# Performance work log

Hardware: AMD Instinct MI355X
Metric: run time of the kernel (lower is better)

The kernel has to match this reference:

```python
import jax, jax.numpy as jnp
import numpy as np

# Model constants (match init_kwargs)
H, P, N, G, NL, K = 32, 64, 128, 1, 15, 4   # heads, head_dim, state, groups, lambda levels, conv width
HID, T, BATCH = 1024, 1024, 1
INTER = H * P                    # 2048
CONV_DIM = INTER + 2 * G * N     # 2304
PROJ = INTER + CONV_DIM + H * (NL + 1)  # 4864
EPS = 1e-5


def _level_matrix(t_len: int) -> np.ndarray:
    """Fenwick-tree level assignment: for query t, prefix [0,t] splits into
    power-of-two segments from binary expansion of t+1; segment of length 2^l -> level l."""
    lm = np.zeros((t_len, t_len), dtype=np.int32)
    for t in range(t_len):
        n = t + 1
        while n > 0:
            lb = n & (-n)
            lm[t, n - lb:n] = lb.bit_length() - 1
            n -= lb
    return lm


def setup_inputs() -> dict:
    key = jax.random.key(0)
    ks = jax.random.split(key, 4)
    return {
        "hidden_states": jax.random.normal(ks[0], (BATCH, T, HID), jnp.float32),
        "in_proj_w": jax.random.normal(ks[1], (PROJ, HID), jnp.float32) / np.sqrt(HID).astype(np.float32),
        "in_proj_b": jnp.zeros((PROJ,), jnp.float32),
        "conv_w": jax.random.normal(ks[2], (CONV_DIM, K), jnp.float32) / np.sqrt(K).astype(np.float32),
        "dt_bias": jnp.ones((H,), jnp.float32),
        "A_log": jnp.log(jnp.arange(1, H + 1, dtype=jnp.float32)),
        "L_param": jnp.ones((H, NL), jnp.float32),
        "D": jnp.ones((H,), jnp.float32),
        "rmsnorm_w": jnp.ones((INTER,), jnp.float32),
        "out_proj_w": jax.random.normal(ks[3], (HID, INTER), jnp.float32) / np.sqrt(INTER).astype(np.float32),
        "out_proj_b": jnp.zeros((HID,), jnp.float32),
        "level_mat": jnp.asarray(_level_matrix(T)),  # (T,T) int32, data-independent
    }


def reference(hidden_states, in_proj_w, in_proj_b, conv_w, dt_bias, A_log,
              L_param, D, rmsnorm_w, out_proj_w, out_proj_b, level_mat):
    b, t, _ = hidden_states.shape
    # in_proj and split: [z | xBC | dt | dl]
    zxbcdtdl = hidden_states @ in_proj_w.T + in_proj_b
    z, xBC, dt, dl = jnp.split(zxbcdtdl, [INTER, INTER + CONV_DIM, INTER + CONV_DIM + H], axis=-1)
    # depthwise causal conv1d (width K) + SiLU
    xp = jnp.pad(xBC, ((0, 0), (K - 1, 0), (0, 0)))
    conv = sum(xp[:, w:w + t, :] * conv_w[:, w] for w in range(K))
    xBC = jax.nn.silu(conv)
    x, Bm, Cm = jnp.split(xBC, [INTER, INTER + G * N], axis=-1)
    x = x.reshape(b, t, H, P)          # v pre-scale
    Bm = Bm.reshape(b, t, G, N)        # keys
    Cm = Cm.reshape(b, t, G, N)        # queries
    dl = dl.reshape(b, t, H, NL)
    # D residual uses unscaled x (matches hmamba_chunk_scan_combined ordering)
    D_res = x * D[None, None, :, None]
    dt = jax.nn.softplus(dt + dt_bias)            # (b,t,H)
    v = x * dt[..., None]                          # (b,t,H,P)
    A = -jnp.exp(A_log)                            # (H,)
    g = A * dt                                     # (b,t,H), per-token log-decay (<=0)
    Ls = jax.nn.softplus(L_param * dl)             # (b,t,H,NL) per-token level scales
    # cumulative log-decay; decay(t,s) = exp(cg_t - cg_s), s<=t
    cg = jnp.cumsum(g, axis=1).transpose(0, 2, 1)  # (b,H,t)
    mask = jnp.tril(jnp.ones((t, t), bool))
    logdecay = jnp.where(mask, cg[:, :, :, None] - cg[:, :, None, :], -jnp.inf)
    decay = jnp.exp(logdecay)                      # (b,H,t,s)
    # hierarchical level scale H[t,s] = Ls[b,t,h, level(t,s)]
    Hmat = jnp.take_along_axis(Ls.transpose(0, 2, 1, 3), level_mat[None, None, :, :], axis=-1)  # (b,H,t,s)
    scores = jnp.einsum('btgn,bsgn->bgts', Cm, Bm)  # (b,G,t,s), G=1 broadcasts over heads
    att = scores * decay * Hmat                     # (b,H,t,s), masked via decay=0
    y = jnp.einsum('bhts,bshp->bthp', att, v) + D_res
    y = y.reshape(b, t, INTER)
    # gated RMSNorm with norm_before_gate=False: normalize(y * silu(z)) * w
    yg = y * jax.nn.silu(z)
    y = yg * jax.lax.rsqrt(jnp.mean(yg * yg, axis=-1, keepdims=True) + EPS) * rmsnorm_w
    return y @ out_proj_w.T + out_proj_b
```

## Files before the change

### kernel.cpp

```cpp
#include <hip/hip_runtime.h>
#include <hip/hip_bf16.h>
#include <math.h>

#define T_LEN 1024
#define HID 1024
#define NHEAD 32
#define HDIM 64
#define NSTATE 128
#define NLVL 15
#define KCONV 4
#define INTER 2048
#define CONV_DIM 2304
#define PROJ 4864
#define EPS 1e-5f

typedef __attribute__((ext_vector_type(8))) _Float16 half8;
typedef __attribute__((ext_vector_type(4))) float float4v;
typedef unsigned short ushort_t;

__device__ __forceinline__ float softplus_f(float x) {
  return fmaxf(x, 0.f) + log1pf(expf(-fabsf(x)));
}
__device__ __forceinline__ float silu_f(float x) {
  return x / (1.f + expf(-x));
}
__device__ __forceinline__ ushort_t f2h(float f) {
  union { _Float16 h; ushort_t u; } v;
  v.h = (_Float16)f;
  return v.u;
}
__device__ __forceinline__ void gload_lds16(const void* g, void* l) {
  __builtin_amdgcn_global_load_lds(
      (const __attribute__((address_space(1))) void*)g,
      (__attribute__((address_space(3))) void*)l, 16, 0, 0);
}

#define N4_HS  (T_LEN * HID / 4)
#define N4_WI  (PROJ * HID / 4)
#define N4_WO  (HID * INTER / 4)
__global__ __launch_bounds__(256) void prep_f16(
    const float* __restrict__ hs, const float* __restrict__ wi,
    const float* __restrict__ wo, ushort_t* __restrict__ hsb,
    ushort_t* __restrict__ wib, ushort_t* __restrict__ wob) {
  int i = blockIdx.x * 256 + threadIdx.x;
  const float* src; ushort_t* dst; int j;
  if (i < N4_HS)              { src = hs; dst = hsb; j = i; }
  else if (i < N4_HS + N4_WI) { src = wi; dst = wib; j = i - N4_HS; }
  else                        { src = wo; dst = wob; j = i - N4_HS - N4_WI; }
  float4 v = reinterpret_cast<const float4*>(src)[j];
  union { ushort_t u[4]; unsigned long long ll; } o;
  o.u[0] = f2h(v.x); o.u[1] = f2h(v.y); o.u[2] = f2h(v.z); o.u[3] = f2h(v.w);
  reinterpret_cast<unsigned long long*>(dst)[j] = o.ll;
}

__global__ __launch_bounds__(256) void gemm_f16_sk(
    const ushort_t* __restrict__ A, const ushort_t* __restrict__ B,
    float* __restrict__ Cpart, int M, int N, int K, int Kc) {
  __shared__ ushort_t As[2][128][32];
  __shared__ ushort_t Bs[2][128][32];
  const int tid = threadIdx.x;
  const int w = tid >> 6, L = tid & 63;
  const int n0 = blockIdx.x * 128, m0 = blockIdx.y * 128;
  const int kbeg = blockIdx.z * Kc;
  float* __restrict__ C = Cpart + (size_t)blockIdx.z * M * N;
  const int mq = (w & 1) * 64, nq = (w >> 1) * 64;
  const int srow = (L >> 2);
  const int sch = (L & 3) * 8;

  float4v acc[4][4];
#pragma unroll
  for (int i = 0; i < 4; ++i)
#pragma unroll
    for (int j = 0; j < 4; ++j) acc[i][j] = (float4v){0.f, 0.f, 0.f, 0.f};

  const int niter = Kc / 32;
  {
    const int kk = kbeg;
#pragma unroll
    for (int j = 0; j < 2; ++j) {
      int r0 = 16 * (w * 2 + j);
      gload_lds16(A + (size_t)(m0 + r0 + srow) * K + kk + sch, &As[0][r0][0]);
      gload_lds16(B + (size_t)(n0 + r0 + srow) * K + kk + sch, &Bs[0][r0][0]);
    }
  }
  for (int it = 0; it < niter; ++it) {
    __syncthreads();
    if (it + 1 < niter) {
      const int kk = kbeg + (it + 1) * 32;
      const int nb = (it + 1) & 1;
#pragma unroll
      for (int j = 0; j < 2; ++j) {
        int r0 = 16 * (w * 2 + j);
        gload_lds16(A + (size_t)(m0 + r0 + srow) * K + kk + sch, &As[nb][r0][0]);
        gload_lds16(B + (size_t)(n0 + r0 + srow) * K + kk + sch, &Bs[nb][r0][0]);
      }
    }
    const int cb = it & 1;
    half8 af[4], bf[4];
#pragma unroll
    for (int t = 0; t < 4; ++t) {
      af[t] = *reinterpret_cast<const half8*>(&As[cb][mq + t * 16 + (L & 15)][(L >> 4) * 8]);
      bf[t] = *reinterpret_cast<const half8*>(&Bs[cb][nq + t * 16 + (L & 15)][(L >> 4) * 8]);
    }
#pragma unroll
    for (int mt = 0; mt < 4; ++mt)
#pragma unroll
      for (int nt = 0; nt < 4; ++nt)
        acc[mt][nt] = __builtin_amdgcn_mfma_f32_16x16x32_f16(af[mt], bf[nt], acc[mt][nt], 0, 0, 0);
  }
  const int qrow = (L >> 4) * 4;
#pragma unroll
  for (int mt = 0; mt < 4; ++mt) {
#pragma unroll
    for (int nt = 0; nt < 4; ++nt) {
      int col = n0 + nq + nt * 16 + (L & 15);
#pragma unroll
      for (int r = 0; r < 4; ++r) {
        int row = m0 + mq + mt * 16 + qrow + r;
        C[(size_t)row * N + col] = acc[mt][nt][r];
      }
    }
  }
}

__global__ __launch_bounds__(256) void reduce_out4(const float* __restrict__ p,
                                                   const float* __restrict__ bias,
                                                   float* __restrict__ out, int MN) {
  int i = blockIdx.x * 256 + threadIdx.x;
  if (i * 4 >= MN) return;
  float4 a = reinterpret_cast<const float4*>(p)[i];
  float4 b = reinterpret_cast<const float4*>(p + MN)[i];
  float4 c = reinterpret_cast<const float4*>(p + 2 * (size_t)MN)[i];
  float4 d = reinterpret_cast<const float4*>(p + 3 * (size_t)MN)[i];
  int col = (i * 4) & (HID - 1);
  float4 bv = *reinterpret_cast<const float4*>(bias + col);
  float4 o;
  o.x = a.x + b.x + c.x + d.x + bv.x;
  o.y = a.y + b.y + c.y + d.y + bv.y;
  o.z = a.z + b.z + c.z + d.z + bv.z;
  o.w = a.w + b.w + c.w + d.w + bv.w;
  reinterpret_cast<float4*>(out)[i] = o;
}

__global__ __launch_bounds__(512) void pointwise_dt(
    const float* __restrict__ zx0, const float* __restrict__ zx1,
    const float* __restrict__ in_b, const float* __restrict__ dt_bias,
    const float* __restrict__ A_log, const float* __restrict__ L_param,
    float* __restrict__ dtbuf, float* __restrict__ gT,
    float* __restrict__ Lsbuf) {
  const int t = blockIdx.x;
  const int j = threadIdx.x;
  const size_t ro = (size_t)t * PROJ;
  if (j < NHEAD * NLVL) {
    int c = INTER + CONV_DIM + NHEAD + j;
    float x = L_param[j] * (zx0[ro + c] + zx1[ro + c] + in_b[c]);
    Lsbuf[(size_t)t * (NHEAD * NLVL) + j] = softplus_f(x);
  } else {
    int h = j - NHEAD * NLVL;
    int c = INTER + CONV_DIM + h;
    float x = zx0[ro + c] + zx1[ro + c] + in_b[c] + dt_bias[h];
    float dt = softplus_f(x);
    dtbuf[t * NHEAD + h] = dt;
    gT[h * T_LEN + t] = -expf(A_log[h]) * dt;
  }
}

__global__ __launch_bounds__(64) void scan_g(const float* __restrict__ gT,
                                             double* __restrict__ cgd) {
  const int h = blockIdx.x, l = threadIdx.x;
  const float* gr = gT + (size_t)h * T_LEN + l * 16;
  double pre[16];
  double acc = 0.0;
#pragma unroll
  for (int i = 0; i < 16; ++i) { acc += (double)gr[i]; pre[i] = acc; }
  double s = acc;
#pragma unroll
  for (int off = 1; off < 64; off <<= 1) {
    double o = __shfl_up(s, off, 64);
    if (l >= off) s += o;
  }
  const double base = s - acc;
  double* cr = cgd + (size_t)h * T_LEN + l * 16;
#pragma unroll
  for (int i = 0; i < 16; ++i) cr[i] = base + pre[i];
}

__global__ __launch_bounds__(256) void conv_fused(
    const float* __restrict__ zx0, const float* __restrict__ zx1,
    const float* __restrict__ in_b, const float* __restrict__ conv_w,
    const float* __restrict__ dtbuf, const float* __restrict__ Dp,
    ushort_t* __restrict__ vt, float* __restrict__ ybuf,
    ushort_t* __restrict__ Bb, ushort_t* __restrict__ Cb) {
  __shared__ ushort_t Vl[64][68];
  __shared__ float dtl[64];
  const int tq = blockIdx.x, cy = blockIdx.y;
  const int t0 = tq * 64;
  const int tid = threadIdx.x;
  const int lane = tid & 63, g = tid >> 6;
  const bool vpath = (cy < 32);
  const int ccol = vpath ? cy * 64 + lane : INTER + (cy - 32) * 64 + lane;
  const int zcol = INTER + ccol;
  float cw[KCONV];
#pragma unroll
  for (int w = 0; w < KCONV; ++w) cw[w] = conv_w[ccol * KCONV + w];
  const float bc = in_b[zcol];
  if (vpath && tid < 64) dtl[tid] = dtbuf[(t0 + tid) * NHEAD + cy];
  const float Dh = vpath ? Dp[cy] : 0.f;

  float xv[19];
#pragma unroll
  for (int i = 0; i < 19; ++i) {
    int tt = t0 + g * 16 - 3 + i;
    if (tt >= 0) {
      size_t o = (size_t)tt * PROJ + zcol;
      xv[i] = zx0[o] + zx1[o] + bc;
    } else xv[i] = 0.f;
  }
  __syncthreads();
#pragma unroll
  for (int i = 0; i < 16; ++i) {
    float acc = xv[i] * cw[0] + xv[i + 1] * cw[1] + xv[i + 2] * cw[2] + xv[i + 3] * cw[3];
    float sil = silu_f(acc);
    int tl = g * 16 + i;
    int t = t0 + tl;
    if (vpath) {
      ushort_t vh = f2h(sil * dtl[tl]);
      Vl[tl][lane] = vh;
      ybuf[(size_t)t * INTER + cy * 64 + lane] = sil * Dh;
    } else if (ccol < INTER + NSTATE) {
      Bb[t * NSTATE + (ccol - INTER)] = f2h(sil);
    } else {
      Cb[t * NSTATE + (ccol - INTER - NSTATE)] = f2h(sil);
    }
  }
  if (vpath) {
    __syncthreads();
#pragma unroll
    for (int rep = 0; rep < 2; ++rep) {
      int u = tid + 256 * rep;
      int p = u >> 3, t8 = (u & 7) * 8;
      union { ushort_t u16[8]; half8 h; } o;
#pragma unroll
      for (int j = 0; j < 8; ++j) o.u16[j] = Vl[t8 + j][p];
      *reinterpret_cast<half8*>(vt + (size_t)(cy * 64 + p) * T_LEN + t0 + t8) = o.h;
    }
  }
}

__global__ __launch_bounds__(256) void attn_mfma(
    const ushort_t* __restrict__ Bb, const ushort_t* __restrict__ Cb,
    const ushort_t* __restrict__ vt, const double* __restrict__ cgd,
    const float* __restrict__ Lsb, float* __restrict__ ybuf) {
  __shared__ ushort_t Bl[64][136];
  __shared__ ushort_t Vtl[64][72];
  __shared__ ushort_t Sl[64][72];
  __shared__ float Lsl[64][16];
  __shared__ float cgq[64];
  __shared__ float cgs[64];

  const int item = blockIdx.x;
  const int h = item / 40;
  const int rem = item - h * 40;
  int qt, j;
  if (rem < 4)        { qt = rem;                 j = 0; }
  else if (rem < 12)  { qt = 4 + (rem - 4) / 2;   j = (rem - 4) % 2; }
  else if (rem < 24)  { qt = 8 + (rem - 12) / 3;  j = (rem - 12) % 3; }
  else                { qt = 12 + (rem - 24) / 4; j = (rem - 24) % 4; }

  const int tid = threadIdx.x;
  const int w = tid >> 6, L = tid & 63;
  const int tq0 = qt * 64;
  const double* cgh = cgd + (size_t)h * T_LEN;
  const double base = cgh[tq0];

  for (int i = tid; i < 64 * NLVL; i += 256) {
    int r = i / NLVL, l = i - r * NLVL;
    Lsl[r][l] = Lsb[(size_t)(tq0 + r) * (NHEAD * NLVL) + h * NLVL + l];
  }
  if (tid < 64) cgq[tid] = (float)(cgh[tq0 + tid] - base);

  half8 cfrag[4];
  {
    const ushort_t* cr = Cb + (size_t)(tq0 + w * 16 + (L & 15)) * NSTATE + (L >> 4) * 8;
#pragma unroll
    for (int ks = 0; ks < 4; ++ks)
      cfrag[ks] = *reinterpret_cast<const half8*>(cr + ks * 32);
  }
  float4v yac[4];
#pragma unroll
  for (int i = 0; i < 4; ++i) yac[i] = (float4v){0.f, 0.f, 0.f, 0.f};

  const int qrow = w * 16 + ((L >> 4) << 2);

  const int st0 = 4 * j;
  const int st1 = min(4 * j + 4, qt + 1);
  for (int st = st0; st < st1; ++st) {
    const int ts0 = st * 64;
    __syncthreads();
#pragma unroll
    for (int i = 0; i < 4; ++i) {
      int u = tid + 256 * i;
      int row = u >> 4, kb = (u & 15) * 8;
      *reinterpret_cast<half8*>(&Bl[row][kb]) =
          *reinterpret_cast<const half8*>(Bb + (size_t)(ts0 + row) * NSTATE + kb);
    }
#pragma unroll
    for (int i = 0; i < 2; ++i) {
      int u = tid + 256 * i;
      int p = u >> 3, sc = (u & 7) * 8;
      *reinterpret_cast<half8*>(&Vtl[p][sc]) =
          *reinterpret_cast<const half8*>(vt + (size_t)(h * HDIM + p) * T_LEN + ts0 + sc);
    }
    if (tid < 64) cgs[tid] = (float)(cgh[ts0 + tid] - base);
    __syncthreads();

    float4v sac[4];
#pragma unroll
    for (int nt = 0; nt < 4; ++nt) sac[nt] = (float4v){0.f, 0.f, 0.f, 0.f};
#pragma unroll
    for (int ks = 0; ks < 4; ++ks) {
#pragma unroll
      for (int nt = 0; nt < 4; ++nt) {
        half8 bfrag = *reinterpret_cast<const half8*>(&Bl[nt * 16 + (L & 15)][ks * 32 + (L >> 4) * 8]);
        sac[nt] = __builtin_amdgcn_mfma_f32_16x16x32_f16(cfrag[ks], bfrag, sac[nt], 0, 0, 0);
      }
    }
#pragma unroll
    for (int nt = 0; nt < 4; ++nt) {
      int s = nt * 16 + (L & 15);
      int sg = ts0 + s;
      float cs = cgs[s];
#pragma unroll
      for (int r = 0; r < 4; ++r) {
        int q = qrow + r;
        int tg = tq0 + q;
        float val = 0.f;
        if (sg <= tg) {
          int lvl = 31 - __clz((unsigned)(sg ^ (tg + 1)));
          val = sac[nt][r] * __expf(cgq[q] - cs) * Lsl[q][lvl];
        }
        Sl[q][s] = f2h(val);
      }
    }
    __builtin_amdgcn_s_waitcnt(0);
#pragma unroll
    for (int ks = 0; ks < 2; ++ks) {
      half8 af = *reinterpret_cast<const half8*>(&Sl[w * 16 + (L & 15)][ks * 32 + (L >> 4) * 8]);
#pragma unroll
      for (int pt = 0; pt < 4; ++pt) {
        half8 bfv = *reinterpret_cast<const half8*>(&Vtl[pt * 16 + (L & 15)][ks * 32 + (L >> 4) * 8]);
        yac[pt] = __builtin_amdgcn_mfma_f32_16x16x32_f16(af, bfv, yac[pt], 0, 0, 0);
      }
    }
  }
#pragma unroll
  for (int pt = 0; pt < 4; ++pt) {
    int p = pt * 16 + (L & 15);
#pragma unroll
    for (int r = 0; r < 4; ++r) {
      int q = qrow + r;
      atomicAdd(ybuf + (size_t)(tq0 + q) * INTER + h * HDIM + p, yac[pt][r]);
    }
  }
}

__global__ __launch_bounds__(256) void rmsnorm_gate(
    const float* __restrict__ ybuf, const float* __restrict__ zx0,
    const float* __restrict__ zx1, const float* __restrict__ in_b,
    const float* __restrict__ w, ushort_t* __restrict__ yhf) {
  __shared__ float red[4];
  const int t = blockIdx.x, tid = threadIdx.x;
  const size_t ro = (size_t)t * PROJ;
  const float* yrow = ybuf + (size_t)t * INTER;
  float yg[8];
  float ss = 0.f;
#pragma unroll
  for (int i = 0; i < 8; ++i) {
    int c = tid + 256 * i;
    float z = zx0[ro + c] + zx1[ro + c] + in_b[c];
    float g = yrow[c] * silu_f(z);
    yg[i] = g;
    ss += g * g;
  }
#pragma unroll
  for (int off = 32; off; off >>= 1) ss += __shfl_down(ss, off, 64);
  if ((tid & 63) == 0) red[tid >> 6] = ss;
  __syncthreads();
  if (tid == 0) red[0] = red[0] + red[1] + red[2] + red[3];
  __syncthreads();
  const float scale = rsqrtf(red[0] / (float)INTER + EPS);
#pragma unroll
  for (int i = 0; i < 8; ++i) {
    int c = tid + 256 * i;
    yhf[(size_t)t * INTER + c] = f2h(yg[i] * scale * w[c]);
  }
}

extern "C" void kernel_launch(void* const* d_in, const int* in_sizes, int n_in,
                              void* d_out, int out_size, void* d_ws, size_t ws_size,
                              hipStream_t stream) {
  const float* hs        = (const float*)d_in[0];
  const float* in_proj_w = (const float*)d_in[1];
  const float* in_proj_b = (const float*)d_in[2];
  const float* conv_w    = (const float*)d_in[3];
  const float* dt_bias   = (const float*)d_in[4];
  const float* A_log     = (const float*)d_in[5];
  const float* L_param   = (const float*)d_in[6];
  const float* Dp        = (const float*)d_in[7];
  const float* rms_w     = (const float*)d_in[8];
  const float* out_proj_w= (const float*)d_in[9];
  const float* out_proj_b= (const float*)d_in[10];
  float* out = (float*)d_out;

  char* W = (char*)d_ws;
  size_t off = 0;
  auto alloc = [&](size_t bytes) { void* p = W + off; off = (off + bytes + 255) & ~(size_t)255; return p; };
  double*   cgd = (double*)  alloc((size_t)NHEAD * T_LEN * 8);
  float*    zx0 = (float*)   alloc((size_t)T_LEN * PROJ * 4);
  float*    zx1 = (float*)   alloc((size_t)T_LEN * PROJ * 4);
  float*    opp = (float*)   alloc((size_t)4 * T_LEN * HID * 4);
  float*    ybuf= (float*)   alloc((size_t)T_LEN * INTER * 4);
  float*    gT  = (float*)   alloc((size_t)NHEAD * T_LEN * 4);
  float*    dtb = (float*)   alloc((size_t)T_LEN * NHEAD * 4);
  float*    Lsb = (float*)   alloc((size_t)T_LEN * NHEAD * NLVL * 4);
  ushort_t* hsb = (ushort_t*)alloc((size_t)T_LEN * HID * 2);
  ushort_t* Wib = (ushort_t*)alloc((size_t)PROJ * HID * 2);
  ushort_t* Wob = (ushort_t*)alloc((size_t)HID * INTER * 2);
  ushort_t* yhf = (ushort_t*)alloc((size_t)T_LEN * INTER * 2);
  ushort_t* vt  = (ushort_t*)alloc((size_t)T_LEN * INTER * 2);
  ushort_t* Bb  = (ushort_t*)alloc((size_t)T_LEN * NSTATE * 2);
  ushort_t* Cb  = (ushort_t*)alloc((size_t)T_LEN * NSTATE * 2);

  prep_f16<<<(N4_HS + N4_WI + N4_WO) / 256, 256, 0, stream>>>(
      hs, in_proj_w, out_proj_w, hsb, Wib, Wob);

  gemm_f16_sk<<<dim3(PROJ / 128, T_LEN / 128, 2), 256, 0, stream>>>(
      hsb, Wib, zx0, T_LEN, PROJ, HID, HID / 2);

  pointwise_dt<<<T_LEN, 512, 0, stream>>>(zx0, zx1, in_proj_b, dt_bias, A_log, L_param,
                                          dtb, gT, Lsb);

  scan_g<<<NHEAD, 64, 0, stream>>>(gT, cgd);

  conv_fused<<<dim3(T_LEN / 64, 36), 256, 0, stream>>>(
      zx0, zx1, in_proj_b, conv_w, dtb, Dp, vt, ybuf, Bb, Cb);

  attn_mfma<<<NHEAD * 40, 256, 0, stream>>>(Bb, Cb, vt, cgd, Lsb, ybuf);

  rmsnorm_gate<<<T_LEN, 256, 0, stream>>>(ybuf, zx0, zx1, in_proj_b, rms_w, yhf);

  gemm_f16_sk<<<dim3(HID / 128, T_LEN / 128, 4), 256, 0, stream>>>(
      yhf, Wob, opp, T_LEN, HID, INTER, INTER / 4);
  reduce_out4<<<(T_LEN * HID / 4 + 255) / 256, 256, 0, stream>>>(
      opp, out_proj_b, out, T_LEN * HID);
}
```

Baseline: 197.7 us.

## Replace split-K input GEMM with single-pass GEMM writing fp16 z/xBC and fp32 dt/dl

The input projection GEMM no longer splits K into two fp32 partial buffers. It now runs a single pass with the bias fused in, writing the z and xBC columns as fp16 and the dt/dl columns as fp32 into a compact buffer. Downstream pointwise, conv and rmsnorm kernels read the pre-reduced, smaller outputs instead of summing two fp32 partials plus bias. This cuts global memory traffic and intermediate storage, but halves the grid of the input GEMM and rounds the z and xBC activations to fp16.

```diff
diff --git a/kernel.cpp b/kernel.cpp
--- a/kernel.cpp
+++ b/kernel.cpp
@@ -12,6 +12,8 @@
 #define INTER 2048
 #define CONV_DIM 2304
 #define PROJ 4864
+#define NPROJ16 4352
+#define NPROJF 512
 #define EPS 1e-5f
 
 typedef __attribute__((ext_vector_type(8))) _Float16 half8;
@@ -28,6 +30,11 @@
   union { _Float16 h; ushort_t u; } v;
   v.h = (_Float16)f;
   return v.u;
+}
+__device__ __forceinline__ float h2f(ushort_t u) {
+  union { ushort_t u; _Float16 h; } v;
+  v.u = u;
+  return (float)v.h;
 }
 __device__ __forceinline__ void gload_lds16(const void* g, void* l) {
   __builtin_amdgcn_global_load_lds(
@@ -51,6 +58,79 @@
   union { ushort_t u[4]; unsigned long long ll; } o;
   o.u[0] = f2h(v.x); o.u[1] = f2h(v.y); o.u[2] = f2h(v.z); o.u[3] = f2h(v.w);
   reinterpret_cast<unsigned long long*>(dst)[j] = o.ll;
+}
+
+__global__ __launch_bounds__(256) void gemm_in(
+    const ushort_t* __restrict__ A, const ushort_t* __restrict__ B,
+    const float* __restrict__ bias,
+    ushort_t* __restrict__ Ch, float* __restrict__ Cf) {
+  const int K = HID;
+  __shared__ ushort_t As[2][128][32];
+  __shared__ ushort_t Bs[2][128][32];
+  const int tid = threadIdx.x;
+  const int w = tid >> 6, L = tid & 63;
+  const int n0 = blockIdx.x * 128, m0 = blockIdx.y * 128;
+  const int mq = (w & 1) * 64, nq = (w >> 1) * 64;
+  const int srow = (L >> 2);
+  const int sch = (L & 3) * 8;
+
+  float4v acc[4][4];
+#pragma unroll
+  for (int i = 0; i < 4; ++i)
+#pragma unroll
+    for (int j = 0; j < 4; ++j) acc[i][j] = (float4v){0.f, 0.f, 0.f, 0.f};
+
+  const int niter = K / 32;
+  {
+#pragma unroll
+    for (int j = 0; j < 2; ++j) {
+      int r0 = 16 * (w * 2 + j);
+      gload_lds16(A + (size_t)(m0 + r0 + srow) * K + sch, &As[0][r0][0]);
+      gload_lds16(B + (size_t)(n0 + r0 + srow) * K + sch, &Bs[0][r0][0]);
+    }
+  }
+  for (int it = 0; it < niter; ++it) {
+    __syncthreads();
+    if (it + 1 < niter) {
+      const int kk = (it + 1) * 32;
+      const int nb = (it + 1) & 1;
+#pragma unroll
+      for (int j = 0; j < 2; ++j) {
+        int r0 = 16 * (w * 2 + j);
+        gload_lds16(A + (size_t)(m0 + r0 + srow) * K + kk + sch, &As[nb][r0][0]);
+        gload_lds16(B + (size_t)(n0 + r0 + srow) * K + kk + sch, &Bs[nb][r0][0]);
+      }
+    }
+    const int cb = it & 1;
+    half8 af[4], bf[4];
+#pragma unroll
+    for (int t = 0; t < 4; ++t) {
+      af[t] = *reinterpret_cast<const half8*>(&As[cb][mq + t * 16 + (L & 15)][(L >> 4) * 8]);
+      bf[t] = *reinterpret_cast<const half8*>(&Bs[cb][nq + t * 16 + (L & 15)][(L >> 4) * 8]);
+    }
+#pragma unroll
+    for (int mt = 0; mt < 4; ++mt)
+#pragma unroll
+      for (int nt = 0; nt < 4; ++nt)
+        acc[mt][nt] = __builtin_amdgcn_mfma_f32_16x16x32_f16(af[mt], bf[nt], acc[mt][nt], 0, 0, 0);
+  }
+  const int qrow = (L >> 4) * 4;
+  const bool tof16 = (n0 < NPROJ16);
+#pragma unroll
+  for (int mt = 0; mt < 4; ++mt) {
+#pragma unroll
+    for (int nt = 0; nt < 4; ++nt) {
+      int col = n0 + nq + nt * 16 + (L & 15);
+      float bv = bias[col];
+#pragma unroll
+      for (int r = 0; r < 4; ++r) {
+        int row = m0 + mq + mt * 16 + qrow + r;
+        float v = acc[mt][nt][r] + bv;
+        if (tof16) Ch[(size_t)row * NPROJ16 + col] = f2h(v);
+        else       Cf[(size_t)row * NPROJF + (col - NPROJ16)] = v;
+      }
+    }
+  }
 }
 
 __global__ __launch_bounds__(256) void gemm_f16_sk(
@@ -143,22 +223,19 @@
 }
 
 __global__ __launch_bounds__(512) void pointwise_dt(
-    const float* __restrict__ zx0, const float* __restrict__ zx1,
-    const float* __restrict__ in_b, const float* __restrict__ dt_bias,
+    const float* __restrict__ zxf, const float* __restrict__ dt_bias,
     const float* __restrict__ A_log, const float* __restrict__ L_param,
     float* __restrict__ dtbuf, float* __restrict__ gT,
     float* __restrict__ Lsbuf) {
   const int t = blockIdx.x;
   const int j = threadIdx.x;
-  const size_t ro = (size_t)t * PROJ;
+  const size_t ro = (size_t)t * NPROJF;
   if (j < NHEAD * NLVL) {
-    int c = INTER + CONV_DIM + NHEAD + j;
-    float x = L_param[j] * (zx0[ro + c] + zx1[ro + c] + in_b[c]);
+    float x = L_param[j] * zxf[ro + NHEAD + j];
     Lsbuf[(size_t)t * (NHEAD * NLVL) + j] = softplus_f(x);
   } else {
     int h = j - NHEAD * NLVL;
-    int c = INTER + CONV_DIM + h;
-    float x = zx0[ro + c] + zx1[ro + c] + in_b[c] + dt_bias[h];
+    float x = zxf[ro + h] + dt_bias[h];
     float dt = softplus_f(x);
     dtbuf[t * NHEAD + h] = dt;
     gT[h * T_LEN + t] = -expf(A_log[h]) * dt;
@@ -186,8 +263,7 @@
 }
 
 __global__ __launch_bounds__(256) void conv_fused(
-    const float* __restrict__ zx0, const float* __restrict__ zx1,
-    const float* __restrict__ in_b, const float* __restrict__ conv_w,
+    const ushort_t* __restrict__ zxh, const float* __restrict__ conv_w,
     const float* __restrict__ dtbuf, const float* __restrict__ Dp,
     ushort_t* __restrict__ vt, float* __restrict__ ybuf,
     ushort_t* __restrict__ Bb, ushort_t* __restrict__ Cb) {
@@ -203,7 +279,6 @@
   float cw[KCONV];
 #pragma unroll
   for (int w = 0; w < KCONV; ++w) cw[w] = conv_w[ccol * KCONV + w];
-  const float bc = in_b[zcol];
   if (vpath && tid < 64) dtl[tid] = dtbuf[(t0 + tid) * NHEAD + cy];
   const float Dh = vpath ? Dp[cy] : 0.f;
 
@@ -212,8 +287,7 @@
   for (int i = 0; i < 19; ++i) {
     int tt = t0 + g * 16 - 3 + i;
     if (tt >= 0) {
-      size_t o = (size_t)tt * PROJ + zcol;
-      xv[i] = zx0[o] + zx1[o] + bc;
+      xv[i] = h2f(zxh[(size_t)tt * NPROJ16 + zcol]);
     } else xv[i] = 0.f;
   }
   __syncthreads();
@@ -365,19 +439,18 @@
 }
 
 __global__ __launch_bounds__(256) void rmsnorm_gate(
-    const float* __restrict__ ybuf, const float* __restrict__ zx0,
-    const float* __restrict__ zx1, const float* __restrict__ in_b,
+    const float* __restrict__ ybuf, const ushort_t* __restrict__ zxh,
     const float* __restrict__ w, ushort_t* __restrict__ yhf) {
   __shared__ float red[4];
   const int t = blockIdx.x, tid = threadIdx.x;
-  const size_t ro = (size_t)t * PROJ;
+  const size_t ro = (size_t)t * NPROJ16;
   const float* yrow = ybuf + (size_t)t * INTER;
   float yg[8];
   float ss = 0.f;
 #pragma unroll
   for (int i = 0; i < 8; ++i) {
     int c = tid + 256 * i;
-    float z = zx0[ro + c] + zx1[ro + c] + in_b[c];
+    float z = h2f(zxh[ro + c]);
     float g = yrow[c] * silu_f(z);
     yg[i] = g;
     ss += g * g;
@@ -416,13 +489,13 @@
   size_t off = 0;
   auto alloc = [&](size_t bytes) { void* p = W + off; off = (off + bytes + 255) & ~(size_t)255; return p; };
   double*   cgd = (double*)  alloc((size_t)NHEAD * T_LEN * 8);
-  float*    zx0 = (float*)   alloc((size_t)T_LEN * PROJ * 4);
-  float*    zx1 = (float*)   alloc((size_t)T_LEN * PROJ * 4);
+  float*    zxf = (float*)   alloc((size_t)T_LEN * NPROJF * 4);
   float*    opp = (float*)   alloc((size_t)4 * T_LEN * HID * 4);
   float*    ybuf= (float*)   alloc((size_t)T_LEN * INTER * 4);
   float*    gT  = (float*)   alloc((size_t)NHEAD * T_LEN * 4);
   float*    dtb = (float*)   alloc((size_t)T_LEN * NHEAD * 4);
   float*    Lsb = (float*)   alloc((size_t)T_LEN * NHEAD * NLVL * 4);
+  ushort_t* zxh = (ushort_t*)alloc((size_t)T_LEN * NPROJ16 * 2);
   ushort_t* hsb = (ushort_t*)alloc((size_t)T_LEN * HID * 2);
   ushort_t* Wib = (ushort_t*)alloc((size_t)PROJ * HID * 2);
   ushort_t* Wob = (ushort_t*)alloc((size_t)HID * INTER * 2);
@@ -434,20 +507,19 @@
   prep_f16<<<(N4_HS + N4_WI + N4_WO) / 256, 256, 0, stream>>>(
       hs, in_proj_w, out_proj_w, hsb, Wib, Wob);
 
-  gemm_f16_sk<<<dim3(PROJ / 128, T_LEN / 128, 2), 256, 0, stream>>>(
-      hsb, Wib, zx0, T_LEN, PROJ, HID, HID / 2);
-
-  pointwise_dt<<<T_LEN, 512, 0, stream>>>(zx0, zx1, in_proj_b, dt_bias, A_log, L_param,
-                                          dtb, gT, Lsb);
+  gemm_in<<<dim3(PROJ / 128, T_LEN / 128), 256, 0, stream>>>(
+      hsb, Wib, in_proj_b, zxh, zxf);
+
+  pointwise_dt<<<T_LEN, 512, 0, stream>>>(zxf, dt_bias, A_log, L_param, dtb, gT, Lsb);
 
   scan_g<<<NHEAD, 64, 0, stream>>>(gT, cgd);
 
   conv_fused<<<dim3(T_LEN / 64, 36), 256, 0, stream>>>(
-      zx0, zx1, in_proj_b, conv_w, dtb, Dp, vt, ybuf, Bb, Cb);
+      zxh, conv_w, dtb, Dp, vt, ybuf, Bb, Cb);
 
   attn_mfma<<<NHEAD * 40, 256, 0, stream>>>(Bb, Cb, vt, cgd, Lsb, ybuf);
 
-  rmsnorm_gate<<<T_LEN, 256, 0, stream>>>(ybuf, zx0, zx1, in_proj_b, rms_w, yhf);
+  rmsnorm_gate<<<T_LEN, 256, 0, stream>>>(ybuf, zxh, rms_w, yhf);
 
   gemm_f16_sk<<<dim3(HID / 128, T_LEN / 128, 4), 256, 0, stream>>>(
       yhf, Wob, opp, T_LEN, HID, INTER, INTER / 4);
```

Result: slower. 206.0 us (+4.2%).
